# Performance work log

Hardware: AMD Instinct MI355X
Metric: run time of the kernel (lower is better)

## Reference

```python
import jax, jax.numpy as jnp
import numpy as np

D_MODEL, N_HEADS = 768, 12
D_K = D_MODEL // N_HEADS
NEG = -1e9


def setup_inputs() -> dict:
    key = jax.random.key(0)
    ks = jax.random.split(key, 12)
    B, S, D = 2, 4096, D_MODEL
    s = 1.0 / np.sqrt(D)
    inp = {
        'query': jax.random.normal(ks[0], (B, S, D), jnp.float32),
        'key': jax.random.normal(ks[1], (B, S, D), jnp.float32),
        'value': jax.random.normal(ks[2], (B, S, D), jnp.float32),
        'mask': jnp.ones((B, S), jnp.int32),
        'Wq': jax.random.normal(ks[3], (D, D), jnp.float32) * s,
        'bq': jnp.zeros((D,), jnp.float32),
        'Wk': jax.random.normal(ks[4], (D, D), jnp.float32) * s,
        'bk': jnp.zeros((D,), jnp.float32),
        'Wv': jax.random.normal(ks[5], (D, D), jnp.float32) * s,
        'bv': jnp.zeros((D,), jnp.float32),
        'Wo': jax.random.normal(ks[6], (D, D), jnp.float32) * s,
        'bo': jnp.zeros((D,), jnp.float32),
    }
    return inp


def reference(query, key, value, mask, Wq, bq, Wk, bk, Wv, bv, Wo, bo):
    B, Sq, D = query.shape
    Sk = key.shape[1]
    # torch Linear: x @ W.T + b; weights stored [out, in]
    def proj(x, W, b, S):
        return (x @ W.T + b).reshape(B, S, N_HEADS, D_K).transpose(0, 2, 1, 3)
    Q = proj(query, Wq, bq, Sq)   # [B,H,Sq,Dk]
    K = proj(key, Wk, bk, Sk)
    V = proj(value, Wv, bv, Sk)
    scores = jnp.einsum('bhqd,bhkd->bhqk', Q, K) / jnp.sqrt(jnp.float32(D_K))
    # padding mask on keys: [B,1,1,Sk]
    scores = jnp.where(mask[:, None, None, :] == 0, NEG, scores)
    # causal mask (triu, diagonal=1)
    causal = jnp.triu(jnp.ones((Sq, Sk), bool), k=1)
    scores = jnp.where(causal[None, None], NEG, scores)
    attn = jax.nn.softmax(scores, axis=-1)
    out = jnp.einsum('bhqk,bhkd->bhqd', attn, V)
    out = out.transpose(0, 2, 1, 3).reshape(B, Sq, D)
    return out @ Wo.T + bo
```

## Files before the change

kernel.cpp:

```cpp
#include <hip/hip_runtime.h>
#include <hip/hip_bf16.h>

#define D_MODEL 768
#define N_HEADS 12
#define D_K     64
#define NEG_INF (-1e9f)
#define SCALE_Q 0.1803368801111154f
#define W_ELEMS (D_MODEL * D_MODEL)

typedef __attribute__((ext_vector_type(8))) short          bf16x8;
typedef __attribute__((ext_vector_type(4))) float          floatx4;
typedef __attribute__((ext_vector_type(4))) unsigned short ushortx4;
typedef __attribute__((ext_vector_type(2))) unsigned int   uintx2;
typedef __attribute__((ext_vector_type(4))) unsigned int   uintx4;

static __device__ __forceinline__ unsigned short f2bf(float f) {
    unsigned u = __builtin_bit_cast(unsigned, f);
    u += 0x7FFFu + ((u >> 16) & 1u);
    return (unsigned short)(u >> 16);
}

static __device__ __forceinline__ void gload_lds16(const void* g, void* l) {
    __builtin_amdgcn_global_load_lds(
        (const __attribute__((address_space(1))) void*)g,
        (__attribute__((address_space(3))) void*)l, 16, 0, 0);
}

__global__ __launch_bounds__(256) void convert_w4(
    const float* __restrict__ W0, const float* __restrict__ W1,
    const float* __restrict__ W2, const float* __restrict__ W3,
    unsigned short* __restrict__ out)
{
    const float* src[4] = {W0, W1, W2, W3};
    const float* W = src[blockIdx.y];
    unsigned short* o = out + (size_t)blockIdx.y * W_ELEMS;
    const int i = (blockIdx.x * 256 + threadIdx.x) * 4;
    float4 v = *(const float4*)(W + i);
    ushortx4 h = { f2bf(v.x), f2bf(v.y), f2bf(v.z), f2bf(v.w) };
    *(ushortx4*)(o + i) = h;
}

__global__ __launch_bounds__(256) void convert_a3(
    const float* __restrict__ A0, const float* __restrict__ A1,
    const float* __restrict__ A2,
    unsigned short* __restrict__ O0, unsigned short* __restrict__ O1,
    unsigned short* __restrict__ O2)
{
    const int z = blockIdx.y;
    const float* A = (z == 0) ? A0 : (z == 1) ? A1 : A2;
    unsigned short* O = (z == 0) ? O0 : (z == 1) ? O1 : O2;
    const int i = (blockIdx.x * 256 + threadIdx.x) * 4;
    float4 v = *(const float4*)(A + i);
    ushortx4 h = { f2bf(v.x), f2bf(v.y), f2bf(v.z), f2bf(v.w) };
    *(ushortx4*)(O + i) = h;
}

template <bool QKV>
__global__ __launch_bounds__(256) void gemm128(
    const unsigned short* __restrict__ A0, const unsigned short* __restrict__ A1,
    const unsigned short* __restrict__ A2,
    const unsigned short* __restrict__ W0, const unsigned short* __restrict__ W1,
    const unsigned short* __restrict__ W2,
    const float* __restrict__ b0, const float* __restrict__ b1,
    const float* __restrict__ b2,
    void* __restrict__ C0, void* __restrict__ C1, void* __restrict__ C2,
    int S)
{
    __shared__ __align__(16) unsigned short As[128 * 32];
    __shared__ __align__(16) unsigned short Bs[128 * 32];

    const int z = QKV ? blockIdx.z : 0;
    const unsigned short* A = (z == 0) ? A0 : (z == 1) ? A1 : A2;
    const unsigned short* W = (z == 0) ? W0 : (z == 1) ? W1 : W2;
    const float* bias       = (z == 0) ? b0 : (z == 1) ? b1 : b2;
    void* C                 = (z == 0) ? C0 : (z == 1) ? C1 : C2;
    const float scale = (QKV && z == 0) ? SCALE_Q : 1.0f;
    const int mode = QKV ? ((z == 2) ? 3 : 1) : 0;

    const int tid  = threadIdx.x;
    const int wave = tid >> 6;
    const int lane = tid & 63;
    const int quad = lane >> 4;
    const int l16  = lane & 15;
    const int m0 = blockIdx.x * 128;
    const int n0 = blockIdx.y * 128;
    const int wm = (wave & 1) * 64;
    const int wn = (wave >> 1) * 64;
    const int sr = lane >> 2;
    const int sc = (lane & 3) << 3;

    const floatx4 zero4 = {0.f, 0.f, 0.f, 0.f};
    floatx4 acc[4][4];
    #pragma unroll
    for (int i = 0; i < 4; ++i)
        #pragma unroll
        for (int j = 0; j < 4; ++j) acc[i][j] = zero4;

    for (int k0 = 0; k0 < D_MODEL; k0 += 32) {
        #pragma unroll
        for (int c = 0; c < 2; ++c) {
            const int row = wave * 32 + c * 16;
            gload_lds16(A + (size_t)(m0 + row + sr) * D_MODEL + k0 + sc,
                        As + row * 32);
            gload_lds16(W + (size_t)(n0 + row + sr) * D_MODEL + k0 + sc,
                        Bs + row * 32);
        }
        __syncthreads();

        bf16x8 af[4], bfr[4];
        #pragma unroll
        for (int i = 0; i < 4; ++i)
            af[i] = *(const bf16x8*)(As + (wm + i * 16 + l16) * 32 + quad * 8);
        #pragma unroll
        for (int j = 0; j < 4; ++j)
            bfr[j] = *(const bf16x8*)(Bs + (wn + j * 16 + l16) * 32 + quad * 8);
        #pragma unroll
        for (int i = 0; i < 4; ++i)
            #pragma unroll
            for (int j = 0; j < 4; ++j)
                acc[i][j] = __builtin_amdgcn_mfma_f32_16x16x32_bf16(
                    bfr[j], af[i], acc[i][j], 0, 0, 0);
        __syncthreads();
    }

    #pragma unroll
    for (int i = 0; i < 4; ++i) {
        const int m = m0 + wm + i * 16 + l16;
        #pragma unroll
        for (int j = 0; j < 4; ++j) {
            const int nb = n0 + wn + j * 16 + quad * 4;
            const float4 bv = *(const float4*)(bias + nb);
            float v0 = (acc[i][j][0] + bv.x) * scale;
            float v1 = (acc[i][j][1] + bv.y) * scale;
            float v2 = (acc[i][j][2] + bv.z) * scale;
            float v3 = (acc[i][j][3] + bv.w) * scale;
            if (mode == 0) {
                float4 o = {v0, v1, v2, v3};
                *(float4*)((float*)C + (size_t)m * D_MODEL + nb) = o;
            } else if (mode == 1) {
                ushortx4 o = {f2bf(v0), f2bf(v1), f2bf(v2), f2bf(v3)};
                *(ushortx4*)((unsigned short*)C + (size_t)m * D_MODEL + nb) = o;
            } else {
                const int bb = m / S, s = m - bb * S;
                const int hh = nb >> 6, d = nb & 63;
                unsigned short* base = (unsigned short*)C +
                    ((size_t)(bb * N_HEADS + hh) * D_K + d) * S + s;
                base[0]         = f2bf(v0);
                base[(size_t)S]     = f2bf(v1);
                base[(size_t)S * 2] = f2bf(v2);
                base[(size_t)S * 3] = f2bf(v3);
            }
        }
    }
}

__global__ __launch_bounds__(256) void flash_attn(
    const unsigned short* __restrict__ Qp,
    const unsigned short* __restrict__ Kp,
    const unsigned short* __restrict__ VpT,
    const int* __restrict__ mask,
    unsigned short* __restrict__ O,
    int S)
{
    __shared__ __align__(16) unsigned short Ks [128 * 64];
    __shared__ __align__(16) unsigned short Vts[64 * 128];
    __shared__ __align__(16) float mskf[128];

    const int L  = blockIdx.x;
    const int bh = L % 24;
    const int p  = L / 24;
    const int h  = bh % 12;
    const int b  = bh / 12;
    const int nqt = S >> 6;
    const int tid  = threadIdx.x;
    const int wave = tid >> 6;
    const int lane = tid & 63;
    const int quad = lane >> 4;
    const int l16  = lane & 15;
    const int sx   = (l16 & 7) << 3;

    const unsigned short* Kbase = Kp  + (size_t)(b * S) * D_MODEL + h * D_K;
    const unsigned short* Vbase = VpT + (size_t)(b * N_HEADS + h) * D_K * S;
    const int* mbase = mask + b * S;

    const int kgrow = wave * 32 + (lane >> 3);
    const int kgcol = ((lane & 7) ^ (lane >> 3)) << 3;
    const int vgrow = wave * 16 + (lane >> 4);
    const int vgc_e = ((lane & 15) ^ (lane >> 4)) << 3;
    const int vgc_o = ((lane & 15) ^ (4 + (lane >> 4))) << 3;

    const floatx4 zero4 = {0.f, 0.f, 0.f, 0.f};
    const short one_bf = (short)0x3F80;
    const bf16x8 ones = {one_bf, one_bf, one_bf, one_bf,
                         one_bf, one_bf, one_bf, one_bf};

    #pragma unroll
    for (int sel = 0; sel < 2; ++sel) {
        const int qt = sel ? (nqt - 1 - p) : p;
        const int q0 = qt * 64;
        const int qbase = q0 + wave * 16;
        const int qabs = qbase + l16;

        const size_t rowQ = (size_t)(b * S + qbase + l16) * D_MODEL + h * D_K;
        const bf16x8 qf0 = *(const bf16x8*)(Qp + rowQ + quad * 8);
        const bf16x8 qf1 = *(const bf16x8*)(Qp + rowQ + 32 + quad * 8);

        floatx4 acc2[4];
        floatx4 acc_l = zero4;
        #pragma unroll
        for (int dt = 0; dt < 4; ++dt) acc2[dt] = zero4;

        const int ni = (qt >> 1) + 1;
        for (int kt = 0; kt < ni; ++kt) {
            const int k0 = kt * 128;
            #pragma unroll
            for (int c = 0; c < 4; ++c) {
                gload_lds16(
                    Kbase + (size_t)(k0 + kgrow + c * 8) * D_MODEL + kgcol,
                    (char*)Ks + (wave * 4 + c) * 1024);
                const int vg = (c & 1) ? vgc_o : vgc_e;
                gload_lds16(
                    Vbase + (size_t)(vgrow + c * 4) * S + k0 + vg,
                    (char*)Vts + (wave * 4 + c) * 1024);
            }
            if (tid < 128)
                mskf[tid] = (mbase[k0 + tid] == 0) ? NEG_INF : 0.f;
            __syncthreads();

            floatx4 s[8];
            #pragma unroll
            for (int nt = 0; nt < 8; ++nt) {
                floatx4 c = *(const floatx4*)(mskf + nt * 16 + quad * 4);
                const unsigned short* kro = Ks + (nt * 16 + l16) * 64;
                bf16x8 kf0 = *(const bf16x8*)(kro + ((quad * 8) ^ sx));
                bf16x8 kf1 = *(const bf16x8*)(kro + ((32 + quad * 8) ^ sx));
                c = __builtin_amdgcn_mfma_f32_16x16x32_bf16(kf0, qf0, c, 0, 0, 0);
                c = __builtin_amdgcn_mfma_f32_16x16x32_bf16(kf1, qf1, c, 0, 0, 0);
                s[nt] = c;
            }

            if (kt == ni - 1) {
                #pragma unroll
                for (int nt = 0; nt < 8; ++nt) {
                    const int kb = k0 + nt * 16 + quad * 4;
                    #pragma unroll
                    for (int r = 0; r < 4; ++r)
                        if (kb + r > qabs) s[nt][r] = NEG_INF;
                }
            }

            unsigned pk0[8], pk1[8];
            #pragma unroll
            for (int nt = 0; nt < 8; ++nt) {
                const float e0 = __builtin_exp2f(s[nt][0]);
                const float e1 = __builtin_exp2f(s[nt][1]);
                const float e2 = __builtin_exp2f(s[nt][2]);
                const float e3 = __builtin_exp2f(s[nt][3]);
                pk0[nt] = __builtin_amdgcn_perm(__builtin_bit_cast(unsigned, e1),
                                                __builtin_bit_cast(unsigned, e0), 0x07060302u);
                pk1[nt] = __builtin_amdgcn_perm(__builtin_bit_cast(unsigned, e3),
                                                __builtin_bit_cast(unsigned, e2), 0x07060302u);
            }

            #pragma unroll
            for (int kh = 0; kh < 4; ++kh) {
                uintx2 a32 = __builtin_amdgcn_permlane32_swap(
                    pk0[2 * kh], pk0[2 * kh + 1], false, false);
                uintx2 b32 = __builtin_amdgcn_permlane32_swap(
                    pk1[2 * kh], pk1[2 * kh + 1], false, false);
                uintx2 a16 = __builtin_amdgcn_permlane16_swap(
                    a32[0], a32[1], false, false);
                uintx2 b16 = __builtin_amdgcn_permlane16_swap(
                    b32[0], b32[1], false, false);
                const uintx4 pw = {a16[0], b16[0], a16[1], b16[1]};
                const bf16x8 pf = __builtin_bit_cast(bf16x8, pw);
                #pragma unroll
                for (int dt = 0; dt < 4; ++dt) {
                    const unsigned short* vro = Vts + (dt * 16 + l16) * 128;
                    bf16x8 vf = *(const bf16x8*)(vro + ((kh * 32 + quad * 8) ^ sx));
                    acc2[dt] = __builtin_amdgcn_mfma_f32_16x16x32_bf16(pf, vf, acc2[dt], 0, 0, 0);
                }
                acc_l = __builtin_amdgcn_mfma_f32_16x16x32_bf16(pf, ones, acc_l, 0, 0, 0);
            }
            __syncthreads();
        }

        #pragma unroll
        for (int r = 0; r < 4; ++r) {
            const float inv = 1.f / acc_l[r];
            const int gq = qbase + quad * 4 + r;
            const size_t base = (size_t)(b * S + gq) * D_MODEL + h * D_K;
            #pragma unroll
            for (int dt = 0; dt < 4; ++dt)
                O[base + dt * 16 + l16] = f2bf(acc2[dt][r] * inv);
        }
        __syncthreads();
    }
}

extern "C" void kernel_launch(void* const* d_in, const int* in_sizes, int n_in,
                              void* d_out, int out_size, void* d_ws, size_t ws_size,
                              hipStream_t stream) {
    const float* query = (const float*)d_in[0];
    const float* key   = (const float*)d_in[1];
    const float* value = (const float*)d_in[2];
    const int*   mask  = (const int*)d_in[3];
    const float* Wq = (const float*)d_in[4];
    const float* bq = (const float*)d_in[5];
    const float* Wk = (const float*)d_in[6];
    const float* bk = (const float*)d_in[7];
    const float* Wv = (const float*)d_in[8];
    const float* bv = (const float*)d_in[9];
    const float* Wo = (const float*)d_in[10];
    const float* bo = (const float*)d_in[11];

    const int B  = 2;
    const int BS = in_sizes[3];
    const int S  = BS / B;
    const int M  = BS;

    unsigned short* Qp  = (unsigned short*)d_ws;
    unsigned short* Kp  = Qp  + (size_t)M * D_MODEL;
    unsigned short* VpT = Kp  + (size_t)M * D_MODEL;
    unsigned short* Obf = VpT + (size_t)M * D_MODEL;
    unsigned short* Wbf = Obf + (size_t)M * D_MODEL;
    unsigned short* Wqb = Wbf;
    unsigned short* Wkb = Wbf + (size_t)W_ELEMS;
    unsigned short* Wvb = Wbf + (size_t)W_ELEMS * 2;
    unsigned short* Wob = Wbf + (size_t)W_ELEMS * 3;
    unsigned short* ka = (unsigned short*)d_out;
    unsigned short* va = ka + (size_t)M * D_MODEL;

    dim3 blk(256);
    convert_w4<<<dim3(W_ELEMS / 1024, 4), blk, 0, stream>>>(Wq, Wk, Wv, Wo, Wbf);
    convert_a3<<<dim3((M * D_MODEL) / 1024, 3), blk, 0, stream>>>(
        query, key, value, Obf, ka, va);

    gemm128<true><<<dim3(M / 128, D_MODEL / 128, 3), blk, 0, stream>>>(
        Obf, ka, va, Wqb, Wkb, Wvb, bq, bk, bv, Qp, Kp, VpT, S);

    flash_attn<<<768, blk, 0, stream>>>(Qp, Kp, VpT, mask, Obf, S);

    gemm128<false><<<dim3(M / 128, D_MODEL / 128, 1), blk, 0, stream>>>(
        Obf, Obf, Obf, Wob, Wob, Wob, bo, bo, bo,
        d_out, d_out, d_out, S);
}
```

Baseline: 306.2 us.

## Double-buffer K/V tiles in flash attention with smaller 64-key tiles

Shrinks the key tile from 128 to 64 rows and double-buffers K, V^T and the mask in LDS, so the loads for the next tile are issued before the current tile's QK/PV MFMAs run. This is meant to hide global-to-LDS latency that previously sat in front of each iteration's compute. The query-tile pairing now hardcodes 63-p instead of nqt-1-p, which only holds for S=4096. The trailing barrier after the output write is also removed. In exchange there are more loop iterations with smaller MFMA batches per barrier.

```diff
diff --git a/kernel.cpp b/kernel.cpp
--- a/kernel.cpp
+++ b/kernel.cpp
@@ -162,9 +162,9 @@
     unsigned short* __restrict__ O,
     int S)
 {
-    __shared__ __align__(16) unsigned short Ks [128 * 64];
-    __shared__ __align__(16) unsigned short Vts[64 * 128];
-    __shared__ __align__(16) float mskf[128];
+    __shared__ __align__(16) unsigned short Ks [2][64 * 64];
+    __shared__ __align__(16) unsigned short Vts[2][64 * 64];
+    __shared__ __align__(16) float mskf[2][64];
 
     const int L  = blockIdx.x;
     const int bh = L % 24;
@@ -183,11 +183,8 @@
     const unsigned short* Vbase = VpT + (size_t)(b * N_HEADS + h) * D_K * S;
     const int* mbase = mask + b * S;
 
-    const int kgrow = wave * 32 + (lane >> 3);
-    const int kgcol = ((lane & 7) ^ (lane >> 3)) << 3;
-    const int vgrow = wave * 16 + (lane >> 4);
-    const int vgc_e = ((lane & 15) ^ (lane >> 4)) << 3;
-    const int vgc_o = ((lane & 15) ^ (4 + (lane >> 4))) << 3;
+    const int srow = wave * 16 + (lane >> 3);
+    const int sgc  = ((lane & 7) ^ (lane >> 3)) << 3;
 
     const floatx4 zero4 = {0.f, 0.f, 0.f, 0.f};
     const short one_bf = (short)0x3F80;
@@ -196,7 +193,7 @@
 
     #pragma unroll
     for (int sel = 0; sel < 2; ++sel) {
-        const int qt = sel ? (nqt - 1 - p) : p;
+        const int qt = sel ? (63 - p) : p;
         const int q0 = qt * 64;
         const int qbase = q0 + wave * 16;
         const int qabs = qbase + l16;
@@ -210,28 +207,43 @@
         #pragma unroll
         for (int dt = 0; dt < 4; ++dt) acc2[dt] = zero4;
 
-        const int ni = (qt >> 1) + 1;
+        const int ni = qt + 1;
+
+        #pragma unroll
+        for (int c = 0; c < 2; ++c) {
+            gload_lds16(Kbase + (size_t)(srow + c * 8) * D_MODEL + sgc,
+                        (char*)Ks[0] + (wave * 2 + c) * 1024);
+            gload_lds16(Vbase + (size_t)(srow + c * 8) * S + sgc,
+                        (char*)Vts[0] + (wave * 2 + c) * 1024);
+        }
+        if (tid < 64) mskf[0][tid] = (mbase[tid] == 0) ? NEG_INF : 0.f;
+        __syncthreads();
+
+        float mr = 0.f;
         for (int kt = 0; kt < ni; ++kt) {
-            const int k0 = kt * 128;
-            #pragma unroll
-            for (int c = 0; c < 4; ++c) {
-                gload_lds16(
-                    Kbase + (size_t)(k0 + kgrow + c * 8) * D_MODEL + kgcol,
-                    (char*)Ks + (wave * 4 + c) * 1024);
-                const int vg = (c & 1) ? vgc_o : vgc_e;
-                gload_lds16(
-                    Vbase + (size_t)(vgrow + c * 4) * S + k0 + vg,
-                    (char*)Vts + (wave * 4 + c) * 1024);
-            }
-            if (tid < 128)
-                mskf[tid] = (mbase[k0 + tid] == 0) ? NEG_INF : 0.f;
-            __syncthreads();
-
-            floatx4 s[8];
-            #pragma unroll
-            for (int nt = 0; nt < 8; ++nt) {
-                floatx4 c = *(const floatx4*)(mskf + nt * 16 + quad * 4);
-                const unsigned short* kro = Ks + (nt * 16 + l16) * 64;
+            const int k0 = kt * 64;
+            const int cur = kt & 1;
+            const bool pre = (kt + 1 < ni);
+
+            if (pre) {
+                const int kn = k0 + 64;
+                #pragma unroll
+                for (int c = 0; c < 2; ++c) {
+                    gload_lds16(
+                        Kbase + (size_t)(kn + srow + c * 8) * D_MODEL + sgc,
+                        (char*)Ks[cur ^ 1] + (wave * 2 + c) * 1024);
+                    gload_lds16(
+                        Vbase + (size_t)(srow + c * 8) * S + kn + sgc,
+                        (char*)Vts[cur ^ 1] + (wave * 2 + c) * 1024);
+                }
+                if (tid < 64) mr = (mbase[kn + tid] == 0) ? NEG_INF : 0.f;
+            }
+
+            floatx4 s[4];
+            #pragma unroll
+            for (int nt = 0; nt < 4; ++nt) {
+                floatx4 c = *(const floatx4*)(&mskf[cur][nt * 16 + quad * 4]);
+                const unsigned short* kro = Ks[cur] + (nt * 16 + l16) * 64;
                 bf16x8 kf0 = *(const bf16x8*)(kro + ((quad * 8) ^ sx));
                 bf16x8 kf1 = *(const bf16x8*)(kro + ((32 + quad * 8) ^ sx));
                 c = __builtin_amdgcn_mfma_f32_16x16x32_bf16(kf0, qf0, c, 0, 0, 0);
@@ -241,7 +253,7 @@
 
             if (kt == ni - 1) {
                 #pragma unroll
-                for (int nt = 0; nt < 8; ++nt) {
+                for (int nt = 0; nt < 4; ++nt) {
                     const int kb = k0 + nt * 16 + quad * 4;
                     #pragma unroll
                     for (int r = 0; r < 4; ++r)
@@ -249,9 +261,9 @@
                 }
             }
 
-            unsigned pk0[8], pk1[8];
-            #pragma unroll
-            for (int nt = 0; nt < 8; ++nt) {
+            unsigned pk0[4], pk1[4];
+            #pragma unroll
+            for (int nt = 0; nt < 4; ++nt) {
                 const float e0 = __builtin_exp2f(s[nt][0]);
                 const float e1 = __builtin_exp2f(s[nt][1]);
                 const float e2 = __builtin_exp2f(s[nt][2]);
@@ -263,7 +275,7 @@
             }
 
             #pragma unroll
-            for (int kh = 0; kh < 4; ++kh) {
+            for (int kh = 0; kh < 2; ++kh) {
                 uintx2 a32 = __builtin_amdgcn_permlane32_swap(
                     pk0[2 * kh], pk0[2 * kh + 1], false, false);
                 uintx2 b32 = __builtin_amdgcn_permlane32_swap(
@@ -276,12 +288,14 @@
                 const bf16x8 pf = __builtin_bit_cast(bf16x8, pw);
                 #pragma unroll
                 for (int dt = 0; dt < 4; ++dt) {
-                    const unsigned short* vro = Vts + (dt * 16 + l16) * 128;
+                    const unsigned short* vro = Vts[cur] + (dt * 16 + l16) * 64;
                     bf16x8 vf = *(const bf16x8*)(vro + ((kh * 32 + quad * 8) ^ sx));
                     acc2[dt] = __builtin_amdgcn_mfma_f32_16x16x32_bf16(pf, vf, acc2[dt], 0, 0, 0);
                 }
                 acc_l = __builtin_amdgcn_mfma_f32_16x16x32_bf16(pf, ones, acc_l, 0, 0, 0);
             }
+
+            if (pre && tid < 64) mskf[cur ^ 1][tid] = mr;
             __syncthreads();
         }
 
@@ -294,7 +308,6 @@
             for (int dt = 0; dt < 4; ++dt)
                 O[base + dt * 16 + l16] = f2bf(acc2[dt][r] * inv);
         }
-        __syncthreads();
     }
 }
 
```

New measurement: 312.9 us. 2.2% more time.
